# Kernel tuning notes

Measured on AMD Instinct MI355X. Metric: run time of the kernel, lower is better.

## Reference

```python
import jax, jax.numpy as jnp
import numpy as np

N_NODES = 100000
N_EDGES = 1600000
IN_DIM, HID_DIM, OUT_DIM = 64, 128, 1


def gcn_conv(x, W, b, src, dst, n_nodes):
    """PyG-style GCNConv: h = x @ W; out = D^-1/2 (A+I) D^-1/2 h + b.
    Self-loops handled analytically (message h_i * dinv_i^2) to avoid
    concatenating them onto the edge list."""
    h = x @ W  # [N, F_out]
    ones = jnp.ones((src.shape[0],), dtype=x.dtype)
    deg = jax.ops.segment_sum(ones, dst, num_segments=n_nodes) + 1.0  # +1 self-loop
    dinv = jax.lax.rsqrt(deg)  # deg >= 1 so always finite
    norm = dinv[src] * dinv[dst]  # [E]
    msgs = h[src] * norm[:, None]  # [E, F_out] gather + scale
    agg = jax.ops.segment_sum(msgs, dst, num_segments=n_nodes)  # scatter-add
    agg = agg + h * (dinv * dinv)[:, None]  # self-loop contribution
    return agg + b


def setup_inputs() -> dict:
    key = jax.random.key(0)
    k1, k2, k3, k4 = jax.random.split(key, 4)
    x = jax.random.normal(k1, (N_NODES, IN_DIM), dtype=jnp.float32)
    edge_index = jax.random.randint(k2, (2, N_EDGES), 0, N_NODES, dtype=jnp.int64)
    # Glorot-ish init for weights
    W1 = jax.random.normal(k3, (IN_DIM, HID_DIM), dtype=jnp.float32) / np.sqrt(IN_DIM)
    b1 = jnp.zeros((HID_DIM,), dtype=jnp.float32)
    W2 = jax.random.normal(k4, (HID_DIM, OUT_DIM), dtype=jnp.float32) / np.sqrt(HID_DIM)
    b2 = jnp.zeros((OUT_DIM,), dtype=jnp.float32)
    return {"x": x, "edge_index": edge_index, "W1": W1, "b1": b1, "W2": W2, "b2": b2}


def reference(x, edge_index, W1, b1, W2, b2):
    src, dst = edge_index[0], edge_index[1]
    h = gcn_conv(x, W1, b1, src, dst, N_NODES)
    h = jax.nn.relu(h)
    # dropout(0.3) in eval mode == identity
    out = gcn_conv(h, W2, b2, src, dst, N_NODES)
    return out.reshape(-1)  # [N]
```

## Files before the change

kernel.cpp:

```cpp
#include <hip/hip_runtime.h>
#include <hip/hip_bf16.h>

#define NNODES 100000
#define NEDGES 1600000
#define IN_DIM 64
#define HID_DIM 128

#define BUKSHIFT 7
#define BUKNODES 128
#define NBUK ((NNODES + 127) >> 7)
#define BUKCAP 2432
#define CHUNK 4096
#define W1TS 72
#define ACCQS 33
#define QS 4096.0f
#define BIAS 32768u

#define EPACK(s, d)  ((s) | (((d) & 127) << 24))
#define ESRC(p)      ((p) & 0x00FFFFFF)
#define EDL(p)       ((int)(((unsigned)(p)) >> 24))

typedef __attribute__((ext_vector_type(8))) short short8;
typedef __attribute__((ext_vector_type(4))) float f32x4;

__device__ inline unsigned short f2bf(float f) {
    unsigned u = __float_as_uint(f);
    u += 0x7fff + ((u >> 16) & 1);
    return (unsigned short)(u >> 16);
}
__device__ inline unsigned bfpack2(float a, float b) {
    return (unsigned)f2bf(a) | ((unsigned)f2bf(b) << 16);
}
__device__ inline int f2i12(float v) {
    float c = fminf(fmaxf(v * QS, -32767.f), 32767.f);
    return __float2int_rn(c);
}
__device__ inline unsigned long long pk64(unsigned w) {
    unsigned lo = (unsigned)((int)(short)(w & 0xffff)) + BIAS;
    unsigned hi = (unsigned)(((int)w) >> 16) + BIAS;
    return ((unsigned long long)hi << 32) | (unsigned long long)lo;
}
__device__ inline unsigned cvt2(int A0, int A1, int s01, float dd) {
    int s0 = (s01 << 16) >> 16, s1 = s01 >> 16;
    return bfpack2((float)(A0 + s0) * dd, (float)(A1 + s1) * dd);
}

__global__ __launch_bounds__(1024, 8) void k_part(const int* __restrict__ src,
                                                  const int* __restrict__ dst,
                                                  int* __restrict__ gbcur,
                                                  int* __restrict__ ebuf, int E) {
    __shared__ int stage[CHUNK];
    __shared__ unsigned short bukof[CHUNK];
    __shared__ int hist[NBUK];
    __shared__ int scanb[NBUK];
    __shared__ int basep[NBUK];
    __shared__ int sb[2][1024];
    int t = threadIdx.x;
    int start = blockIdx.x * CHUNK;
    int n = E - start; if (n > CHUNK) n = CHUNK;

    if (t < NBUK) hist[t] = 0;
    __syncthreads();

    int myb[4], myr[4], mp[4];
    #pragma unroll
    for (int i = 0; i < 4; i++) {
        int c = t + i * 1024;
        if (c < n) {
            int s = src[start + c];
            int d = dst[start + c];
            int b = d >> BUKSHIFT;
            myb[i] = b;
            mp[i]  = EPACK(s, d);
            myr[i] = atomicAdd(&hist[b], 1);
        } else myb[i] = -1;
    }
    __syncthreads();

    {
        int v = (t < NBUK) ? hist[t] : 0;
        sb[0][t] = v;
        __syncthreads();
        int pin = 0;
        for (int ofs = 1; ofs < 1024; ofs <<= 1) {
            sb[pin ^ 1][t] = (t >= ofs) ? sb[pin][t] + sb[pin][t - ofs] : sb[pin][t];
            __syncthreads();
            pin ^= 1;
        }
        if (t < NBUK) scanb[t] = sb[pin][t] - v;
    }

    if (t < NBUK) {
        int h = hist[t];
        basep[t] = h ? (t * BUKCAP + atomicAdd(&gbcur[t], h)) : 0;
    }
    __syncthreads();

    #pragma unroll
    for (int i = 0; i < 4; i++) {
        if (myb[i] >= 0) {
            int p = scanb[myb[i]] + myr[i];
            stage[p] = mp[i];
            bukof[p] = (unsigned short)myb[i];
        }
    }
    __syncthreads();

    for (int c = t; c < n; c += 1024) {
        int b = bukof[c];
        ebuf[basep[b] + (c - scanb[b])] = stage[c];
    }
}

__global__ __launch_bounds__(1024, 8) void k_bfill(const int* __restrict__ gbcur,
                                                   const int* __restrict__ ebuf,
                                                   const float* __restrict__ x,
                                                   int* __restrict__ off,
                                                   int* __restrict__ nend,
                                                   float* __restrict__ dinv,
                                                   int* __restrict__ csr,
                                                   short* __restrict__ xsq, int N) {
    __shared__ int sEdge[BUKCAP];
    __shared__ int lcnt[BUKNODES];
    __shared__ int sbuf[2][BUKNODES];
    __shared__ int cur[BUKNODES];
    __shared__ float sdinv[BUKNODES];
    int b = blockIdx.x, t = threadIdx.x;
    int nbase = b << BUKSHIFT;
    int rbase = b * BUKCAP;
    int cntb = gbcur[b];
    if (t < BUKNODES) lcnt[t] = 0;
    __syncthreads();
    for (int i = t; i < cntb; i += 1024) {
        int p = ebuf[rbase + i];
        sEdge[i] = p;
        atomicAdd(&lcnt[EDL(p)], 1);
    }
    __syncthreads();
    int v = (t < BUKNODES) ? lcnt[t] : 0;
    if (t < BUKNODES) sbuf[0][t] = v;
    __syncthreads();
    int pin = 0;
    for (int ofs = 1; ofs < BUKNODES; ofs <<= 1) {
        if (t < BUKNODES) sbuf[pin ^ 1][t] = (t >= ofs) ? sbuf[pin][t] + sbuf[pin][t - ofs]
                                                        : sbuf[pin][t];
        __syncthreads();
        pin ^= 1;
    }
    if (t < BUKNODES) {
        int o = rbase + sbuf[pin][t] - v;
        int nid = nbase + t;
        float dv = rsqrtf((float)v + 1.0f);
        sdinv[t] = dv;
        if (nid < N) {
            off[nid]  = o;
            nend[nid] = o + v;
            dinv[nid] = dv;
        }
        cur[t] = o;
    }
    __syncthreads();
    for (int i = t; i < cntb; i += 1024) {
        int p = sEdge[i];
        int pos = atomicAdd(&cur[EDL(p)], 1);
        csr[pos] = ESRC(p);
    }
    for (int i = t; i < BUKNODES * 16; i += 1024) {
        int nl = i >> 4;
        int nid = nbase + nl;
        if (nid < N) {
            float dv = sdinv[nl];
            float4 vx = ((const float4*)x)[(size_t)nid * 16 + (i & 15)];
            int q0 = f2i12(vx.x * dv), q1 = f2i12(vx.y * dv);
            int q2 = f2i12(vx.z * dv), q3 = f2i12(vx.w * dv);
            uint2 u;
            u.x = (q0 & 0xffff) | (q1 << 16);
            u.y = (q2 & 0xffff) | (q3 << 16);
            ((uint2*)xsq)[(size_t)nid * 16 + (i & 15)] = u;
        }
    }
}

__global__ __launch_bounds__(512, 6) void k_aggmlp(const int* __restrict__ gbcur,
                                                   const int* __restrict__ ebuf,
                                                   const short* __restrict__ xsq,
                                                   const int* __restrict__ off,
                                                   const int* __restrict__ nend,
                                                   const float* __restrict__ dinv,
                                                   const float* __restrict__ W1,
                                                   const float* __restrict__ b1,
                                                   const float* __restrict__ W2,
                                                   float* __restrict__ zd, int N) {
    __shared__ unsigned long long accq[BUKNODES * ACCQS];
    __shared__ __align__(16) unsigned short sW1t[HID_DIM * W1TS];
    __shared__ float sW2[HID_DIM];
    __shared__ float sb1[HID_DIM];
    int b = blockIdx.x, t = threadIdx.x;
    int rbase = b * BUKCAP;
    int cntb = gbcur[b];

    for (int i = t; i < BUKNODES * ACCQS; i += 512) accq[i] = 0ULL;
    for (int i = t; i < IN_DIM * HID_DIM; i += 512) {
        int k = i >> 7, hid = i & 127;
        sW1t[hid * W1TS + k] = f2bf(W1[i]);
    }
    if (t < HID_DIM) { sW2[t] = W2[t]; sb1[t] = b1[t]; }
    __syncthreads();

    int c = t & 7;
    int g = t >> 3;
    const uint4* xq4 = (const uint4*)xsq;

    int cp0 = 0, cp1 = 0; bool cv0 = false, cv1 = false;
    uint4 cua = {0, 0, 0, 0}, cub = {0, 0, 0, 0};
    if (cntb > 0) {
        int e0 = g, e1 = 64 + g;
        cv0 = e0 < cntb; cv1 = e1 < cntb;
        cp0 = cv0 ? ebuf[rbase + e0] : 0;
        cp1 = cv1 ? ebuf[rbase + e1] : 0;
        if (cv0) cua = xq4[(size_t)ESRC(cp0) * 8 + c];
        if (cv1) cub = xq4[(size_t)ESRC(cp1) * 8 + c];
    }
    for (int base = 0; base < cntb; base += 128) {
        int nb = base + 128;
        int np0 = 0, np1 = 0; bool nv0 = false, nv1 = false;
        uint4 nua = {0, 0, 0, 0}, nub = {0, 0, 0, 0};
        if (nb < cntb) {
            int e0 = nb + g, e1 = nb + 64 + g;
            nv0 = e0 < cntb; nv1 = e1 < cntb;
            np0 = nv0 ? ebuf[rbase + e0] : 0;
            np1 = nv1 ? ebuf[rbase + e1] : 0;
            if (nv0) nua = xq4[(size_t)ESRC(np0) * 8 + c];
            if (nv1) nub = xq4[(size_t)ESRC(np1) * 8 + c];
        }
        if (cv0) {
            unsigned long long* ar = &accq[EDL(cp0) * ACCQS + c];
            atomicAdd(&ar[0],  pk64(cua.x));
            atomicAdd(&ar[8],  pk64(cua.y));
            atomicAdd(&ar[16], pk64(cua.z));
            atomicAdd(&ar[24], pk64(cua.w));
        }
        if (cv1) {
            unsigned long long* ar = &accq[EDL(cp1) * ACCQS + c];
            atomicAdd(&ar[0],  pk64(cub.x));
            atomicAdd(&ar[8],  pk64(cub.y));
            atomicAdd(&ar[16], pk64(cub.z));
            atomicAdd(&ar[24], pk64(cub.w));
        }
        cp0 = np0; cp1 = np1; cv0 = nv0; cv1 = nv1; cua = nua; cub = nub;
    }
    __syncthreads();

    int w = t >> 6, lane = t & 63;
    int col = lane & 15, quad = lane >> 4;
    int node0 = b << BUKSHIFT;
    int na = node0 + w * 16 + col;
    int nac = na < N ? na : N - 1;
    float dd = dinv[nac] * (1.0f / QS);
    int deg = nend[nac] - off[nac];
    unsigned ub = (unsigned)deg * BIAS;

    int nl = w * 16 + col;
    const unsigned long long* arow = &accq[nl * ACCQS];
    uint4 s0 = xq4[(size_t)nac * 8 + quad];
    uint4 s1 = xq4[(size_t)nac * 8 + 4 + quad];
    union { unsigned u[4]; short8 v; } A0, A1;
    #pragma unroll
    for (int k = 0; k < 4; k++) {
        unsigned long long q0 = arow[k * 8 + quad];
        unsigned long long q1 = arow[k * 8 + 4 + quad];
        int lo0 = (int)((unsigned)(q0 & 0xffffffffULL) - ub);
        int hi0 = (int)((unsigned)(q0 >> 32) - ub);
        int lo1 = (int)((unsigned)(q1 & 0xffffffffULL) - ub);
        int hi1 = (int)((unsigned)(q1 >> 32) - ub);
        unsigned sp0 = (k == 0) ? s0.x : (k == 1) ? s0.y : (k == 2) ? s0.z : s0.w;
        unsigned sp1 = (k == 0) ? s1.x : (k == 1) ? s1.y : (k == 2) ? s1.z : s1.w;
        A0.u[k] = cvt2(lo0, hi0, (int)sp0, dd);
        A1.u[k] = cvt2(lo1, hi1, (int)sp1, dd);
    }

    float zpart[4] = {0, 0, 0, 0};
    #pragma unroll
    for (int h0 = 0; h0 < 8; h0++) {
        int hid = h0 * 16 + col;
        const short8* brow = (const short8*)(sW1t + hid * W1TS);
        short8 b0 = brow[quad];
        short8 b1f = brow[4 + quad];
        f32x4 cc = {0.f, 0.f, 0.f, 0.f};
        cc = __builtin_amdgcn_mfma_f32_16x16x32_bf16(A0.v, b0, cc, 0, 0, 0);
        cc = __builtin_amdgcn_mfma_f32_16x16x32_bf16(A1.v, b1f, cc, 0, 0, 0);
        float bb = sb1[hid], ww = sW2[hid];
        #pragma unroll
        for (int r = 0; r < 4; r++) {
            float v = cc[r] + bb;
            zpart[r] += (v > 0.f ? v : 0.f) * ww;
        }
    }
    #pragma unroll
    for (int m = 1; m < 16; m <<= 1) {
        #pragma unroll
        for (int r = 0; r < 4; r++) zpart[r] += __shfl_xor(zpart[r], m);
    }
    if (col == 0) {
        #pragma unroll
        for (int r = 0; r < 4; r++) {
            int n = node0 + w * 16 + quad * 4 + r;
            if (n < N) zd[n] = zpart[r] * dinv[n];
        }
    }
}

__global__ __launch_bounds__(1024, 8) void k_gather1(const int* __restrict__ off,
                                                     const int* __restrict__ nend,
                                                     const int* __restrict__ csr,
                                                     const float* __restrict__ zd,
                                                     const float* __restrict__ dinv,
                                                     const float* __restrict__ b2,
                                                     float* __restrict__ out, int n_nodes) {
    int tid = blockIdx.x * 1024 + threadIdx.x;
    int n = tid >> 3;
    int l = tid & 7;
    if (n >= n_nodes) return;
    int beg = off[n], fin = nend[n];
    float a0 = 0.0f, a1 = 0.0f;
    for (int i = beg + l; i < fin; i += 16) {
        a0 += zd[csr[i]];
        int i2 = i + 8;
        if (i2 < fin) a1 += zd[csr[i2]];
    }
    float a = a0 + a1;
    a += __shfl_xor(a, 1);
    a += __shfl_xor(a, 2);
    a += __shfl_xor(a, 4);
    if (l == 0) out[n] = (a + zd[n]) * dinv[n] + b2[0];
}

extern "C" void kernel_launch(void* const* d_in, const int* in_sizes, int n_in,
                              void* d_out, int out_size, void* d_ws, size_t ws_size,
                              hipStream_t stream) {
    const float* x  = (const float*)d_in[0];
    const int*   ei = (const int*)d_in[1];
    const float* W1 = (const float*)d_in[2];
    const float* b1 = (const float*)d_in[3];
    const float* W2 = (const float*)d_in[4];
    const float* b2 = (const float*)d_in[5];
    float* out = (float*)d_out;

    const int N = NNODES;
    const int E = NEDGES;
    const int* src = ei;
    const int* dst = ei + E;

    int* gbcur = (int*)d_ws;
    int* off   = gbcur + 1024;
    int* nend  = off + N;
    float* dinv = (float*)(nend + N);
    float* zd   = dinv + N;
    int* csr    = (int*)(zd + N);
    size_t o1 = ((size_t)((char*)(csr + NBUK * BUKCAP) - (char*)d_ws) + 127) & ~(size_t)127;
    short* xsq = (short*)((char*)d_ws + o1);
    size_t o2 = o1 + (size_t)N * 128;
    int* ebuf  = (int*)((char*)d_ws + o2);

    hipMemsetAsync(gbcur, 0, 1024 * sizeof(int), stream);
    k_part<<<(E + CHUNK - 1) / CHUNK, 1024, 0, stream>>>(src, dst, gbcur, ebuf, E);
    k_bfill<<<NBUK, 1024, 0, stream>>>(gbcur, ebuf, x, off, nend, dinv, csr, xsq, N);
    k_aggmlp<<<NBUK, 512, 0, stream>>>(gbcur, ebuf, xsq, off, nend, dinv, W1, b1, W2, zd, N);
    k_gather1<<<(N * 8 + 1023) / 1024, 1024, 0, stream>>>(off, nend, csr, zd, dinv, b2, out, N);
}
```

Measured before the change: 172.7 us.

## Deepen software pipeline of edge gather and LDS atomic accumulation

Restructures the per-bucket edge aggregation loop into a three-stage pipeline. Edge words are loaded two iterations ahead, feature rows one iteration ahead, and atomics run on the current batch. Each thread now handles 4 edges per iteration instead of 2. This puts more gather loads in flight to hide global memory latency, at the cost of more registers and possibly lower occupancy.

```diff
diff --git a/kernel.cpp b/kernel.cpp
--- a/kernel.cpp
+++ b/kernel.cpp
@@ -211,43 +211,50 @@
     int g = t >> 3;
     const uint4* xq4 = (const uint4*)xsq;
 
-    int cp0 = 0, cp1 = 0; bool cv0 = false, cv1 = false;
-    uint4 cua = {0, 0, 0, 0}, cub = {0, 0, 0, 0};
-    if (cntb > 0) {
-        int e0 = g, e1 = 64 + g;
-        cv0 = e0 < cntb; cv1 = e1 < cntb;
-        cp0 = cv0 ? ebuf[rbase + e0] : 0;
-        cp1 = cv1 ? ebuf[rbase + e1] : 0;
-        if (cv0) cua = xq4[(size_t)ESRC(cp0) * 8 + c];
-        if (cv1) cub = xq4[(size_t)ESRC(cp1) * 8 + c];
-    }
-    for (int base = 0; base < cntb; base += 128) {
-        int nb = base + 128;
-        int np0 = 0, np1 = 0; bool nv0 = false, nv1 = false;
-        uint4 nua = {0, 0, 0, 0}, nub = {0, 0, 0, 0};
-        if (nb < cntb) {
-            int e0 = nb + g, e1 = nb + 64 + g;
-            nv0 = e0 < cntb; nv1 = e1 < cntb;
-            np0 = nv0 ? ebuf[rbase + e0] : 0;
-            np1 = nv1 ? ebuf[rbase + e1] : 0;
-            if (nv0) nua = xq4[(size_t)ESRC(np0) * 8 + c];
-            if (nv1) nub = xq4[(size_t)ESRC(np1) * 8 + c];
-        }
-        if (cv0) {
-            unsigned long long* ar = &accq[EDL(cp0) * ACCQS + c];
-            atomicAdd(&ar[0],  pk64(cua.x));
-            atomicAdd(&ar[8],  pk64(cua.y));
-            atomicAdd(&ar[16], pk64(cua.z));
-            atomicAdd(&ar[24], pk64(cua.w));
-        }
-        if (cv1) {
-            unsigned long long* ar = &accq[EDL(cp1) * ACCQS + c];
-            atomicAdd(&ar[0],  pk64(cub.x));
-            atomicAdd(&ar[8],  pk64(cub.y));
-            atomicAdd(&ar[16], pk64(cub.z));
-            atomicAdd(&ar[24], pk64(cub.w));
-        }
-        cp0 = np0; cp1 = np1; cv0 = nv0; cv1 = nv1; cua = nua; cub = nub;
+    int w0[4], w1[4], w2[4];
+    bool v0[4], v1[4], v2[4];
+    uint4 r0[4], r1[4];
+
+    auto LW = [&](int B, int* W, bool* V) {
+        #pragma unroll
+        for (int j = 0; j < 4; j++) {
+            int e = B + j * 64 + g;
+            V[j] = e < cntb;
+            W[j] = V[j] ? ebuf[rbase + e] : 0;
+        }
+    };
+    auto LR = [&](const int* W, const bool* V, uint4* R) {
+        #pragma unroll
+        for (int j = 0; j < 4; j++) {
+            uint4 z = {0, 0, 0, 0};
+            R[j] = V[j] ? xq4[(size_t)ESRC(W[j]) * 8 + c] : z;
+        }
+    };
+    auto AT = [&](const int* W, const bool* V, const uint4* R) {
+        #pragma unroll
+        for (int j = 0; j < 4; j++) {
+            if (V[j]) {
+                unsigned long long* ar = &accq[EDL(W[j]) * ACCQS + c];
+                atomicAdd(&ar[0],  pk64(R[j].x));
+                atomicAdd(&ar[8],  pk64(R[j].y));
+                atomicAdd(&ar[16], pk64(R[j].z));
+                atomicAdd(&ar[24], pk64(R[j].w));
+            }
+        }
+    };
+
+    LW(0, w0, v0);
+    LW(256, w1, v1);
+    LR(w0, v0, r0);
+    for (int base = 0; base < cntb; base += 256) {
+        LR(w1, v1, r1);
+        LW(base + 512, w2, v2);
+        AT(w0, v0, r0);
+        #pragma unroll
+        for (int j = 0; j < 4; j++) {
+            w0[j] = w1[j]; v0[j] = v1[j]; r0[j] = r1[j];
+            w1[j] = w2[j]; v1[j] = v2[j];
+        }
     }
     __syncthreads();
 
```

Result: slower. 190.0 us (+10.0%).
